# Kernel tuning notes

Hardware: AMD Instinct MI355X
Metric: run time of the kernel (lower is better)

Reference implementation:

```python
import jax, jax.numpy as jnp
import numpy as np

H, N_FULL, L_KERNEL, CHANNELS, RANK = 256, 128, 2048, 1, 1


def _legs_nplr(N, rank=1):
    # HiPPO-LegS transition + rank-1 correction -> NPLR (diag w - P P^*) form.
    q = np.arange(N, dtype=np.float64)
    col, row = np.meshgrid(q, q)
    r = 2 * q + 1
    M = -(np.where(row >= col, r, 0) - np.diag(q))
    T = np.sqrt(np.diag(2 * q + 1))
    A = T @ M @ np.linalg.inv(T)
    B = np.diag(T)                        # (N,)
    P = np.sqrt(0.5 + q)[None, :]         # (rank=1, N)
    AP = A + (P[:, :, None] * P[:, None, :]).sum(0)
    w, V = np.linalg.eig(AP)              # complex eigendecomposition
    w = w[0::2]                           # keep one of each conjugate pair -> N//2
    V = V[:, 0::2]
    V_inv = V.conj().T
    Bc = V_inv @ B.astype(V.dtype)        # (N//2,)
    Pc = (V_inv @ P.T.astype(V.dtype)).T  # (rank, N//2)
    return w, Pc, Bc


def _c2r(a):
    return jnp.stack([jnp.real(a), jnp.imag(a)], axis=-1).astype(jnp.float32)


def _r2c(a):
    return jax.lax.complex(a[..., 0], a[..., 1])


def setup_inputs() -> dict:
    key = jax.random.key(0)
    k1, k2 = jax.random.split(key)
    w, P, B = _legs_nplr(N_FULL, RANK)    # numpy complex128, half-size N = 64
    Nh = w.shape[-1]
    w = jnp.asarray(np.broadcast_to(w[None, :], (H, Nh)).copy())
    P = jnp.asarray(np.broadcast_to(P[:, None, :], (RANK, H, Nh)).copy())
    B = jnp.asarray(np.broadcast_to(B[None, None, :], (1, H, Nh)).copy())
    C = jax.random.normal(k1, (CHANNELS, H, Nh, 2), dtype=jnp.float32)
    log_dt = jax.random.uniform(k2, (H,), dtype=jnp.float32) * (
        float(np.log(0.1)) - float(np.log(0.001))) + float(np.log(0.001))
    return {
        'w_ri': _c2r(w), 'P_ri': _c2r(P), 'B_ri': _c2r(B),
        'C_ri': C, 'log_dt': log_dt, 'L': L_KERNEL,
    }


def reference(w_ri, P_ri, B_ri, C_ri, log_dt, L):
    w = _r2c(w_ri)        # (H, N) complex64
    P = _r2c(P_ri)        # (r, H, N)
    B = _r2c(B_ri)        # (1, H, N)
    C = _r2c(C_ri)        # (c, H, N)
    dt = jnp.exp(log_dt)  # (H,)
    Lh = L // 2 + 1
    # FFT nodes, processed through the bilinear transform
    omega = jnp.exp((-2j * np.pi / L) * jnp.arange(Lh, dtype=jnp.float32))
    z = 2 * (1 - omega) / (1 + omega)
    w_dt = w * dt[:, None]                               # incorporate dt into A
    Bcat = jnp.concatenate([B, P], axis=0)               # (1+r, H, N)
    Ccat = jnp.concatenate([C, jnp.conj(P)], axis=0)     # (c+r, H, N)  Q = conj(P)
    v = Bcat[:, None] * Ccat[None]                       # (1+r, c+r, H, N)
    # conjugate-symmetric extension to the full 2N poles
    v2 = jnp.concatenate([v, jnp.conj(v)], axis=-1)      # (1+r, c+r, H, 2N)
    w2 = jnp.concatenate([w_dt, jnp.conj(w_dt)], axis=-1)  # (H, 2N)
    # naive Cauchy sum (the O(N*L) hotspot): (1+r, c+r, H, Lh)
    r = (v2[..., None] / (z - w2[..., None])).sum(axis=-2)
    r = r * dt[None, None, :, None]
    # rank-1 Woodbury correction for the low-rank term
    k_f = r[:-1, :-1] - r[:-1, -1:] * r[-1:, :-1] / (1 + r[-1:, -1:])
    # final bilinear-transform correction, then frequency -> time
    k_f = k_f * 2 / (1 + omega)
    k = jnp.fft.irfft(k_f, n=L, axis=-1)                 # (1, c, H, L) real
    return k[0].astype(jnp.float32)                      # (c, H, L)
```

## Files before the change

### kernel.cpp

```cpp
#include <hip/hip_runtime.h>

#define NH 64
#define LFULL 2048
#define MH 1024
#define PI_F 3.14159265358979323846f
#define ANG_HALF 1.5339807878856412e-3f
#define ANG_3A   3.0679615757712823e-3f
#define ANG_FFT  6.1359231515425647e-3f

typedef __attribute__((ext_vector_type(2))) float f32x2;
typedef __attribute__((ext_vector_type(4))) float f32x4;

#define SV2(v, i, j) __builtin_shufflevector((v), (v), (i), (j))

#define ONE_POLE(SEL, pna, pm2, pa00, pb00, pa01, pb01, pa10, pb10, pa11, pb11) do { \
    f32x2 dr, di;                                                                    \
    asm("v_pk_add_f32 %0, %1, %2 op_sel:[" SEL ",0] op_sel_hi:[" SEL ",1]"           \
        : "=v"(dr) : "v"(pm2), "v"(nyy2));                                           \
    asm("v_pk_mul_f32 %0, %1, %2 op_sel:[" SEL ",0] op_sel_hi:[" SEL ",1]"           \
        : "=v"(di) : "v"(pna), "v"(yp));                                             \
    const f32x2 den = dr*dr + di*di;                                                 \
    const float pprod = den.x * den.y;                                               \
    const float ipp = __builtin_amdgcn_rcpf(pprod);                                  \
    f32x2 t;  t.x = ipp * den.y;  t.y = ipp * den.x;                                 \
    const f32x2 U = dr * t;                                                          \
    const f32x2 V = di * t;                                                          \
    asm("v_pk_fma_f32 %0, %1, %2, %0 op_sel:[" SEL ",0,0] op_sel_hi:[" SEL ",1,1]"   \
        : "+v"(s1_00) : "v"(pa00), "v"(U));                                          \
    asm("v_pk_fma_f32 %0, %1, %2, %0 op_sel:[" SEL ",0,0] op_sel_hi:[" SEL ",1,1]"   \
        : "+v"(s2_00) : "v"(pa00), "v"(V));                                          \
    asm("v_pk_fma_f32 %0, %1, %2, %0 op_sel:[" SEL ",0,0] op_sel_hi:[" SEL ",1,1]"   \
        : "+v"(s3_00) : "v"(pb00), "v"(U));                                          \
    asm("v_pk_fma_f32 %0, %1, %2, %0 op_sel:[" SEL ",0,0] op_sel_hi:[" SEL ",1,1]"   \
        : "+v"(s4_00) : "v"(pb00), "v"(V));                                          \
    asm("v_pk_fma_f32 %0, %1, %2, %0 op_sel:[" SEL ",0,0] op_sel_hi:[" SEL ",1,1]"   \
        : "+v"(s1_01) : "v"(pa01), "v"(U));                                          \
    asm("v_pk_fma_f32 %0, %1, %2, %0 op_sel:[" SEL ",0,0] op_sel_hi:[" SEL ",1,1]"   \
        : "+v"(s2_01) : "v"(pa01), "v"(V));                                          \
    asm("v_pk_fma_f32 %0, %1, %2, %0 op_sel:[" SEL ",0,0] op_sel_hi:[" SEL ",1,1]"   \
        : "+v"(s3_01) : "v"(pb01), "v"(U));                                          \
    asm("v_pk_fma_f32 %0, %1, %2, %0 op_sel:[" SEL ",0,0] op_sel_hi:[" SEL ",1,1]"   \
        : "+v"(s4_01) : "v"(pb01), "v"(V));                                          \
    asm("v_pk_fma_f32 %0, %1, %2, %0 op_sel:[" SEL ",0,0] op_sel_hi:[" SEL ",1,1]"   \
        : "+v"(s1_10) : "v"(pa10), "v"(U));                                          \
    asm("v_pk_fma_f32 %0, %1, %2, %0 op_sel:[" SEL ",0,0] op_sel_hi:[" SEL ",1,1]"   \
        : "+v"(s2_10) : "v"(pa10), "v"(V));                                          \
    asm("v_pk_fma_f32 %0, %1, %2, %0 op_sel:[" SEL ",0,0] op_sel_hi:[" SEL ",1,1]"   \
        : "+v"(s3_10) : "v"(pb10), "v"(U));                                          \
    asm("v_pk_fma_f32 %0, %1, %2, %0 op_sel:[" SEL ",0,0] op_sel_hi:[" SEL ",1,1]"   \
        : "+v"(s4_10) : "v"(pb10), "v"(V));                                          \
    asm("v_pk_fma_f32 %0, %1, %2, %0 op_sel:[" SEL ",0,0] op_sel_hi:[" SEL ",1,1]"   \
        : "+v"(s1_11) : "v"(pa11), "v"(U));                                          \
    asm("v_pk_fma_f32 %0, %1, %2, %0 op_sel:[" SEL ",0,0] op_sel_hi:[" SEL ",1,1]"   \
        : "+v"(s2_11) : "v"(pa11), "v"(V));                                          \
    asm("v_pk_fma_f32 %0, %1, %2, %0 op_sel:[" SEL ",0,0] op_sel_hi:[" SEL ",1,1]"   \
        : "+v"(s3_11) : "v"(pb11), "v"(U));                                          \
    asm("v_pk_fma_f32 %0, %1, %2, %0 op_sel:[" SEL ",0,0] op_sel_hi:[" SEL ",1,1]"   \
        : "+v"(s4_11) : "v"(pb11), "v"(V));                                          \
} while (0)

__global__ __launch_bounds__(512) void hippo_ssk(
    const float* __restrict__ w_ri,
    const float* __restrict__ P_ri,
    const float* __restrict__ B_ri,
    const float* __restrict__ C_ri,
    const float* __restrict__ log_dt,
    float* __restrict__ out)
{
    __shared__ __attribute__((aligned(16))) float coeff[10][NH];
    __shared__ float2 Kf[MH + 1];
    __shared__ float2 bufA[MH];
    __shared__ float2 bufB[MH];

    const int h    = blockIdx.x;
    const int tid  = threadIdx.x;
    const int c    = tid & 255;
    const int eps  = tid >> 8;

    float2 w_, P_, B_, C_;  float dtv = 0.f;
    if (tid < NH) {
        dtv = log_dt[h];
        w_ = ((const float2*)w_ri)[h*NH + tid];
        P_ = ((const float2*)P_ri)[h*NH + tid];
        B_ = ((const float2*)B_ri)[h*NH + tid];
        C_ = ((const float2*)C_ri)[h*NH + tid];
    }

    float shA, chA, shB, chB;
    __sincosf(ANG_HALF * (float)tid,         &shA, &chA);
    __sincosf(ANG_HALF * (float)(tid + 512), &shB, &chB);
    const float yA = 2.f * shA * __builtin_amdgcn_rcpf(chA);
    const float yB = 2.f * shB * __builtin_amdgcn_rcpf(chB);
    f32x2 yp;   yp.x = yA;        yp.y = yB;
    f32x2 nyy2; nyy2.x = -yA*yA;  nyy2.y = -yB*yB;
    float sa, ca;
    __sincosf(ANG_3A * (float)tid, &sa, &ca);
    const float cw0 = ca*ca - sa*sa;
    const float sw0 = 2.f*ca*sa;
    float w1c[4], w1s[4];
    #pragma unroll
    for (int mi = 0; mi < 4; ++mi) {
        const int m = 2 << (2*mi);
        __sincosf(ANG_FFT * (float)(c & ~(m-1)), &w1s[mi], &w1c[mi]);
    }

    if (tid < NH) {
        const float dt = __expf(dtv);
        const float a = w_.x * dt, b = w_.y * dt;
        const float v00r = (B_.x*C_.x - B_.y*C_.y) * dt;
        const float v00i = (B_.x*C_.y + B_.y*C_.x) * dt;
        const float v01r = (B_.x*P_.x + B_.y*P_.y) * dt;
        const float v01i = (B_.y*P_.x - B_.x*P_.y) * dt;
        const float v10r = (P_.x*C_.x - P_.y*C_.y) * dt;
        const float v10i = (P_.x*C_.y + P_.y*C_.x) * dt;
        const float v11  = (P_.x*P_.x + P_.y*P_.y) * dt;
        coeff[0][tid] = -2.f*a;
        coeff[1][tid] = fmaf(a, a, b*b);
        coeff[2][tid] = -2.f*fmaf(v00r, a, v00i*b);
        coeff[3][tid] = 2.f*v00r;
        coeff[4][tid] = -2.f*fmaf(v01r, a, v01i*b);
        coeff[5][tid] = 2.f*v01r;
        coeff[6][tid] = -2.f*fmaf(v10r, a, v10i*b);
        coeff[7][tid] = 2.f*v10r;
        coeff[8][tid] = -2.f*v11*a;
        coeff[9][tid] = 2.f*v11;
        float s = v00r;
        #pragma unroll
        for (int off = 32; off > 0; off >>= 1) s += __shfl_down(s, off, 64);
        if (tid == 0) Kf[MH] = make_float2(s, 0.f);
    }
    __syncthreads();

    {
        f32x2 s1_00={0,0}, s2_00={0,0}, s3_00={0,0}, s4_00={0,0};
        f32x2 s1_01={0,0}, s2_01={0,0}, s3_01={0,0}, s4_01={0,0};
        f32x2 s1_10={0,0}, s2_10={0,0}, s3_10={0,0}, s4_10={0,0};
        f32x2 s1_11={0,0}, s2_11={0,0}, s3_11={0,0}, s4_11={0,0};
        #pragma unroll 2
        for (int n = 0; n < NH; n += 4) {
            const f32x4 q0 = *reinterpret_cast<const f32x4*>(&coeff[0][n]);
            const f32x4 q1 = *reinterpret_cast<const f32x4*>(&coeff[1][n]);
            const f32x4 q2 = *reinterpret_cast<const f32x4*>(&coeff[2][n]);
            const f32x4 q3 = *reinterpret_cast<const f32x4*>(&coeff[3][n]);
            const f32x4 q4 = *reinterpret_cast<const f32x4*>(&coeff[4][n]);
            const f32x4 q5 = *reinterpret_cast<const f32x4*>(&coeff[5][n]);
            const f32x4 q6 = *reinterpret_cast<const f32x4*>(&coeff[6][n]);
            const f32x4 q7 = *reinterpret_cast<const f32x4*>(&coeff[7][n]);
            const f32x4 q8 = *reinterpret_cast<const f32x4*>(&coeff[8][n]);
            const f32x4 q9 = *reinterpret_cast<const f32x4*>(&coeff[9][n]);
            {
                const f32x2 pna = SV2(q0,0,1), pm2 = SV2(q1,0,1);
                const f32x2 pa00 = SV2(q2,0,1), pb00 = SV2(q3,0,1);
                const f32x2 pa01 = SV2(q4,0,1), pb01 = SV2(q5,0,1);
                const f32x2 pa10 = SV2(q6,0,1), pb10 = SV2(q7,0,1);
                const f32x2 pa11 = SV2(q8,0,1), pb11 = SV2(q9,0,1);
                ONE_POLE("0", pna, pm2, pa00, pb00, pa01, pb01, pa10, pb10, pa11, pb11);
                ONE_POLE("1", pna, pm2, pa00, pb00, pa01, pb01, pa10, pb10, pa11, pb11);
            }
            {
                const f32x2 pna = SV2(q0,2,3), pm2 = SV2(q1,2,3);
                const f32x2 pa00 = SV2(q2,2,3), pb00 = SV2(q3,2,3);
                const f32x2 pa01 = SV2(q4,2,3), pb01 = SV2(q5,2,3);
                const f32x2 pa10 = SV2(q6,2,3), pb10 = SV2(q7,2,3);
                const f32x2 pa11 = SV2(q8,2,3), pb11 = SV2(q9,2,3);
                ONE_POLE("0", pna, pm2, pa00, pb00, pa01, pb01, pa10, pb10, pa11, pb11);
                ONE_POLE("1", pna, pm2, pa00, pb00, pa01, pb01, pa10, pb10, pa11, pb11);
            }
        }
        const f32x2 r00r = yp*s4_00 + s1_00;
        const f32x2 r00i = yp*s3_00 - s2_00;
        const f32x2 r01r = yp*s4_01 + s1_01;
        const f32x2 r01i = yp*s3_01 - s2_01;
        const f32x2 r10r = yp*s4_10 + s1_10;
        const f32x2 r10i = yp*s3_10 - s2_10;
        const f32x2 r11r = yp*s4_11 + s1_11;
        const f32x2 r11i = yp*s3_11 - s2_11;
        const f32x2 nr = r01r*r10r - r01i*r10i;
        const f32x2 ni = r01r*r10i + r01i*r10r;
        const f32x2 dw = 1.f + r11r;
        const f32x2 dv = r11i;
        const f32x2 d2 = dw*dw + dv*dv;
        f32x2 id2;
        id2.x = __builtin_amdgcn_rcpf(d2.x);
        id2.y = __builtin_amdgcn_rcpf(d2.y);
        const f32x2 cr = (nr*dw + ni*dv)*id2;
        const f32x2 ci = (ni*dw - nr*dv)*id2;
        const f32x2 k0r = r00r - cr;
        const f32x2 k0i = r00i - ci;
        const f32x2 hy = 0.5f*yp;
        Kf[tid]       = make_float2(k0r.x - k0i.x*hy.x, k0i.x + k0r.x*hy.x);
        Kf[tid + 512] = make_float2(k0r.y - k0i.y*hy.y, k0i.y + k0r.y*hy.y);
    }
    __syncthreads();

    {
        float2 Xk = Kf[tid];
        if (tid == 0) Xk.y = 0.f;
        float2 Xc = Kf[MH - tid];  Xc.y = -Xc.y;
        const float Er0 = 0.5f*(Xk.x + Xc.x), Ei0 = 0.5f*(Xk.y + Xc.y);
        const float Tr0 = 0.5f*(Xk.x - Xc.x), Ti0 = 0.5f*(Xk.y - Xc.y);
        const float2 Z0 = make_float2(Er0 - (ca*Ti0 + sa*Tr0), Ei0 + (ca*Tr0 - sa*Ti0));
        const float2 Xk1 = Kf[tid + 512];
        float2 Xc1 = Kf[512 - tid];  Xc1.y = -Xc1.y;
        const float Er1 = 0.5f*(Xk1.x + Xc1.x), Ei1 = 0.5f*(Xk1.y + Xc1.y);
        const float Tr1 = 0.5f*(Xk1.x - Xc1.x), Ti1 = 0.5f*(Xk1.y - Xc1.y);
        const float Or1 = -sa*Tr1 - ca*Ti1;
        const float Oi1 = -sa*Ti1 + ca*Tr1;
        const float2 Z1 = make_float2(Er1 - Oi1, Ei1 + Or1);
        const float drr = Z0.x - Z1.x, dii = Z0.y - Z1.y;
        float4 outv;
        outv.x = Z0.x + Z1.x;
        outv.y = Z0.y + Z1.y;
        outv.z = cw0*drr - sw0*dii;
        outv.w = cw0*dii + sw0*drr;
        *reinterpret_cast<float4*>(&bufA[2*tid]) = outv;
    }
    __syncthreads();

    float2* Xb = bufA;
    float2* Yb = bufB;
    #pragma unroll
    for (int mi = 0; mi < 4; ++mi) {
        const int m   = 2 << (2*mi);
        const int jm1 = c & ~(m - 1);
        const int r   = c & (m - 1);
        const float c1v = w1c[mi], s1 = w1s[mi];
        const float2 x0 = Xb[c];
        const float2 x1 = Xb[c + 256];
        const float2 x2 = Xb[c + 512];
        const float2 x3 = Xb[c + 768];
        const float2 s02 = make_float2(x0.x + x2.x, x0.y + x2.y);
        const float2 d02 = make_float2(x0.x - x2.x, x0.y - x2.y);
        const float2 s13 = make_float2(x1.x + x3.x, x1.y + x3.y);
        const float2 d13 = make_float2(x1.x - x3.x, x1.y - x3.y);
        const float2 wd02 = make_float2(c1v*d02.x - s1*d02.y, c1v*d02.y + s1*d02.x);
        const float2 wd13 = make_float2(-s1*d13.x - c1v*d13.y, c1v*d13.x - s1*d13.y);
        const float2 Yu = eps ? wd02 : s02;
        const float2 Yv = eps ? wd13 : s13;
        const float Wc = c1v*c1v - s1*s1;
        const float Ws = 2.f*c1v*s1;
        const float2 Zp = make_float2(Yu.x + Yv.x, Yu.y + Yv.y);
        const float2 Zd = make_float2(Yu.x - Yv.x, Yu.y - Yv.y);
        const int p = 4*jm1 + (eps ? m : 0) + r;
        Yb[p]       = Zp;
        Yb[p + 2*m] = make_float2(Wc*Zd.x - Ws*Zd.y, Wc*Zd.y + Ws*Zd.x);
        __syncthreads();
        float2* t = Xb; Xb = Yb; Yb = t;
    }

    {
        const float sc = 1.0f/1024.0f;
        float2* op2 = (float2*)(out + (size_t)h * LFULL);
        const float2 a0 = Xb[tid];
        const float2 a1 = Xb[tid + 512];
        op2[tid]       = make_float2((a0.x + a1.x)*sc, (a0.y + a1.y)*sc);
        op2[tid + 512] = make_float2((a0.x - a1.x)*sc, (a0.y - a1.y)*sc);
    }
}

extern "C" void kernel_launch(void* const* d_in, const int* in_sizes, int n_in,
                              void* d_out, int out_size, void* d_ws, size_t ws_size,
                              hipStream_t stream) {
    const float* w_ri   = (const float*)d_in[0];
    const float* P_ri   = (const float*)d_in[1];
    const float* B_ri   = (const float*)d_in[2];
    const float* C_ri   = (const float*)d_in[3];
    const float* log_dt = (const float*)d_in[4];
    float* out = (float*)d_out;
    const int Hn = in_sizes[4];
    hippo_ssk<<<dim3(Hn), dim3(512), 0, stream>>>(w_ri, P_ri, B_ri, C_ri, log_dt, out);
}
```

Before: 15.69 us.

## Compute four frequencies per thread in Cauchy loop using half the block

The Cauchy sum is now done by only the first 256 threads, each handling four frequency nodes (two packed pairs) instead of two. Each coefficient LDS load is reused across twice as many frequencies, halving shared-memory read traffic for the pole loop. In exchange, half the block's waves sit idle during the dominant phase and per-thread register pressure doubles (64 accumulator registers), which may cut occupancy or cause spills. The loop unroll pragma is also dropped.

After: 21.12 us. 1.35x slower.

```diff
diff --git a/kernel.cpp b/kernel.cpp
--- a/kernel.cpp
+++ b/kernel.cpp
@@ -13,12 +13,12 @@
 
 #define SV2(v, i, j) __builtin_shufflevector((v), (v), (i), (j))
 
-#define ONE_POLE(SEL, pna, pm2, pa00, pb00, pa01, pb01, pa10, pb10, pa11, pb11) do { \
+#define ONE_POLE_G(SEL, G, YP, NYY2) do {                                            \
     f32x2 dr, di;                                                                    \
     asm("v_pk_add_f32 %0, %1, %2 op_sel:[" SEL ",0] op_sel_hi:[" SEL ",1]"           \
-        : "=v"(dr) : "v"(pm2), "v"(nyy2));                                           \
+        : "=v"(dr) : "v"(pm2), "v"(NYY2));                                           \
     asm("v_pk_mul_f32 %0, %1, %2 op_sel:[" SEL ",0] op_sel_hi:[" SEL ",1]"           \
-        : "=v"(di) : "v"(pna), "v"(yp));                                             \
+        : "=v"(di) : "v"(pna), "v"(YP));                                             \
     const f32x2 den = dr*dr + di*di;                                                 \
     const float pprod = den.x * den.y;                                               \
     const float ipp = __builtin_amdgcn_rcpf(pprod);                                  \
@@ -26,37 +26,63 @@
     const f32x2 U = dr * t;                                                          \
     const f32x2 V = di * t;                                                          \
     asm("v_pk_fma_f32 %0, %1, %2, %0 op_sel:[" SEL ",0,0] op_sel_hi:[" SEL ",1,1]"   \
-        : "+v"(s1_00) : "v"(pa00), "v"(U));                                          \
-    asm("v_pk_fma_f32 %0, %1, %2, %0 op_sel:[" SEL ",0,0] op_sel_hi:[" SEL ",1,1]"   \
-        : "+v"(s2_00) : "v"(pa00), "v"(V));                                          \
-    asm("v_pk_fma_f32 %0, %1, %2, %0 op_sel:[" SEL ",0,0] op_sel_hi:[" SEL ",1,1]"   \
-        : "+v"(s3_00) : "v"(pb00), "v"(U));                                          \
-    asm("v_pk_fma_f32 %0, %1, %2, %0 op_sel:[" SEL ",0,0] op_sel_hi:[" SEL ",1,1]"   \
-        : "+v"(s4_00) : "v"(pb00), "v"(V));                                          \
-    asm("v_pk_fma_f32 %0, %1, %2, %0 op_sel:[" SEL ",0,0] op_sel_hi:[" SEL ",1,1]"   \
-        : "+v"(s1_01) : "v"(pa01), "v"(U));                                          \
-    asm("v_pk_fma_f32 %0, %1, %2, %0 op_sel:[" SEL ",0,0] op_sel_hi:[" SEL ",1,1]"   \
-        : "+v"(s2_01) : "v"(pa01), "v"(V));                                          \
-    asm("v_pk_fma_f32 %0, %1, %2, %0 op_sel:[" SEL ",0,0] op_sel_hi:[" SEL ",1,1]"   \
-        : "+v"(s3_01) : "v"(pb01), "v"(U));                                          \
-    asm("v_pk_fma_f32 %0, %1, %2, %0 op_sel:[" SEL ",0,0] op_sel_hi:[" SEL ",1,1]"   \
-        : "+v"(s4_01) : "v"(pb01), "v"(V));                                          \
-    asm("v_pk_fma_f32 %0, %1, %2, %0 op_sel:[" SEL ",0,0] op_sel_hi:[" SEL ",1,1]"   \
-        : "+v"(s1_10) : "v"(pa10), "v"(U));                                          \
-    asm("v_pk_fma_f32 %0, %1, %2, %0 op_sel:[" SEL ",0,0] op_sel_hi:[" SEL ",1,1]"   \
-        : "+v"(s2_10) : "v"(pa10), "v"(V));                                          \
-    asm("v_pk_fma_f32 %0, %1, %2, %0 op_sel:[" SEL ",0,0] op_sel_hi:[" SEL ",1,1]"   \
-        : "+v"(s3_10) : "v"(pb10), "v"(U));                                          \
-    asm("v_pk_fma_f32 %0, %1, %2, %0 op_sel:[" SEL ",0,0] op_sel_hi:[" SEL ",1,1]"   \
-        : "+v"(s4_10) : "v"(pb10), "v"(V));                                          \
-    asm("v_pk_fma_f32 %0, %1, %2, %0 op_sel:[" SEL ",0,0] op_sel_hi:[" SEL ",1,1]"   \
-        : "+v"(s1_11) : "v"(pa11), "v"(U));                                          \
-    asm("v_pk_fma_f32 %0, %1, %2, %0 op_sel:[" SEL ",0,0] op_sel_hi:[" SEL ",1,1]"   \
-        : "+v"(s2_11) : "v"(pa11), "v"(V));                                          \
-    asm("v_pk_fma_f32 %0, %1, %2, %0 op_sel:[" SEL ",0,0] op_sel_hi:[" SEL ",1,1]"   \
-        : "+v"(s3_11) : "v"(pb11), "v"(U));                                          \
-    asm("v_pk_fma_f32 %0, %1, %2, %0 op_sel:[" SEL ",0,0] op_sel_hi:[" SEL ",1,1]"   \
-        : "+v"(s4_11) : "v"(pb11), "v"(V));                                          \
+        : "+v"(s1_00##G) : "v"(pa00), "v"(U));                                       \
+    asm("v_pk_fma_f32 %0, %1, %2, %0 op_sel:[" SEL ",0,0] op_sel_hi:[" SEL ",1,1]"   \
+        : "+v"(s2_00##G) : "v"(pa00), "v"(V));                                       \
+    asm("v_pk_fma_f32 %0, %1, %2, %0 op_sel:[" SEL ",0,0] op_sel_hi:[" SEL ",1,1]"   \
+        : "+v"(s3_00##G) : "v"(pb00), "v"(U));                                       \
+    asm("v_pk_fma_f32 %0, %1, %2, %0 op_sel:[" SEL ",0,0] op_sel_hi:[" SEL ",1,1]"   \
+        : "+v"(s4_00##G) : "v"(pb00), "v"(V));                                       \
+    asm("v_pk_fma_f32 %0, %1, %2, %0 op_sel:[" SEL ",0,0] op_sel_hi:[" SEL ",1,1]"   \
+        : "+v"(s1_01##G) : "v"(pa01), "v"(U));                                       \
+    asm("v_pk_fma_f32 %0, %1, %2, %0 op_sel:[" SEL ",0,0] op_sel_hi:[" SEL ",1,1]"   \
+        : "+v"(s2_01##G) : "v"(pa01), "v"(V));                                       \
+    asm("v_pk_fma_f32 %0, %1, %2, %0 op_sel:[" SEL ",0,0] op_sel_hi:[" SEL ",1,1]"   \
+        : "+v"(s3_01##G) : "v"(pb01), "v"(U));                                       \
+    asm("v_pk_fma_f32 %0, %1, %2, %0 op_sel:[" SEL ",0,0] op_sel_hi:[" SEL ",1,1]"   \
+        : "+v"(s4_01##G) : "v"(pb01), "v"(V));                                       \
+    asm("v_pk_fma_f32 %0, %1, %2, %0 op_sel:[" SEL ",0,0] op_sel_hi:[" SEL ",1,1]"   \
+        : "+v"(s1_10##G) : "v"(pa10), "v"(U));                                       \
+    asm("v_pk_fma_f32 %0, %1, %2, %0 op_sel:[" SEL ",0,0] op_sel_hi:[" SEL ",1,1]"   \
+        : "+v"(s2_10##G) : "v"(pa10), "v"(V));                                       \
+    asm("v_pk_fma_f32 %0, %1, %2, %0 op_sel:[" SEL ",0,0] op_sel_hi:[" SEL ",1,1]"   \
+        : "+v"(s3_10##G) : "v"(pb10), "v"(U));                                       \
+    asm("v_pk_fma_f32 %0, %1, %2, %0 op_sel:[" SEL ",0,0] op_sel_hi:[" SEL ",1,1]"   \
+        : "+v"(s4_10##G) : "v"(pb10), "v"(V));                                       \
+    asm("v_pk_fma_f32 %0, %1, %2, %0 op_sel:[" SEL ",0,0] op_sel_hi:[" SEL ",1,1]"   \
+        : "+v"(s1_11##G) : "v"(pa11), "v"(U));                                       \
+    asm("v_pk_fma_f32 %0, %1, %2, %0 op_sel:[" SEL ",0,0] op_sel_hi:[" SEL ",1,1]"   \
+        : "+v"(s2_11##G) : "v"(pa11), "v"(V));                                       \
+    asm("v_pk_fma_f32 %0, %1, %2, %0 op_sel:[" SEL ",0,0] op_sel_hi:[" SEL ",1,1]"   \
+        : "+v"(s3_11##G) : "v"(pb11), "v"(U));                                       \
+    asm("v_pk_fma_f32 %0, %1, %2, %0 op_sel:[" SEL ",0,0] op_sel_hi:[" SEL ",1,1]"   \
+        : "+v"(s4_11##G) : "v"(pb11), "v"(V));                                       \
+} while (0)
+
+#define FINISH_G(G, YP, L0, L1) do {                                                 \
+    const f32x2 r00r = (YP)*s4_00##G + s1_00##G;                                     \
+    const f32x2 r00i = (YP)*s3_00##G - s2_00##G;                                     \
+    const f32x2 r01r = (YP)*s4_01##G + s1_01##G;                                     \
+    const f32x2 r01i = (YP)*s3_01##G - s2_01##G;                                     \
+    const f32x2 r10r = (YP)*s4_10##G + s1_10##G;                                     \
+    const f32x2 r10i = (YP)*s3_10##G - s2_10##G;                                     \
+    const f32x2 r11r = (YP)*s4_11##G + s1_11##G;                                     \
+    const f32x2 r11i = (YP)*s3_11##G - s2_11##G;                                     \
+    const f32x2 nr = r01r*r10r - r01i*r10i;                                          \
+    const f32x2 ni = r01r*r10i + r01i*r10r;                                          \
+    const f32x2 dw = 1.f + r11r;                                                     \
+    const f32x2 dv = r11i;                                                           \
+    const f32x2 d2 = dw*dw + dv*dv;                                                  \
+    f32x2 id2;                                                                       \
+    id2.x = __builtin_amdgcn_rcpf(d2.x);                                             \
+    id2.y = __builtin_amdgcn_rcpf(d2.y);                                             \
+    const f32x2 cr = (nr*dw + ni*dv)*id2;                                            \
+    const f32x2 ci = (ni*dw - nr*dv)*id2;                                            \
+    const f32x2 k0r = r00r - cr;                                                     \
+    const f32x2 k0i = r00i - ci;                                                     \
+    const f32x2 hy = 0.5f*(YP);                                                      \
+    Kf[(L0)] = make_float2(k0r.x - k0i.x*hy.x, k0i.x + k0r.x*hy.x);                  \
+    Kf[(L1)] = make_float2(k0r.y - k0i.y*hy.y, k0i.y + k0r.y*hy.y);                  \
 } while (0)
 
 __global__ __launch_bounds__(512) void hippo_ssk(
@@ -86,13 +112,20 @@
         C_ = ((const float2*)C_ri)[h*NH + tid];
     }
 
-    float shA, chA, shB, chB;
-    __sincosf(ANG_HALF * (float)tid,         &shA, &chA);
-    __sincosf(ANG_HALF * (float)(tid + 512), &shB, &chB);
-    const float yA = 2.f * shA * __builtin_amdgcn_rcpf(chA);
-    const float yB = 2.f * shB * __builtin_amdgcn_rcpf(chB);
-    f32x2 yp;   yp.x = yA;        yp.y = yB;
-    f32x2 nyy2; nyy2.x = -yA*yA;  nyy2.y = -yB*yB;
+    f32x2 ypA, nyy2A, ypB, nyy2B;
+    {
+        float sh0, ch0, sh1, ch1, sh2, ch2, sh3, ch3;
+        __sincosf(ANG_HALF * (float)c,         &sh0, &ch0);
+        __sincosf(ANG_HALF * (float)(c + 512), &sh1, &ch1);
+        __sincosf(ANG_HALF * (float)(c + 256), &sh2, &ch2);
+        __sincosf(ANG_HALF * (float)(c + 768), &sh3, &ch3);
+        const float y0 = 2.f * sh0 * __builtin_amdgcn_rcpf(ch0);
+        const float y1 = 2.f * sh1 * __builtin_amdgcn_rcpf(ch1);
+        const float y2 = 2.f * sh2 * __builtin_amdgcn_rcpf(ch2);
+        const float y3 = 2.f * sh3 * __builtin_amdgcn_rcpf(ch3);
+        ypA.x = y0;  ypA.y = y1;  nyy2A.x = -y0*y0;  nyy2A.y = -y1*y1;
+        ypB.x = y2;  ypB.y = y3;  nyy2B.x = -y2*y2;  nyy2B.y = -y3*y3;
+    }
     float sa, ca;
     __sincosf(ANG_3A * (float)tid, &sa, &ca);
     const float cw0 = ca*ca - sa*sa;
@@ -131,12 +164,15 @@
     }
     __syncthreads();
 
-    {
-        f32x2 s1_00={0,0}, s2_00={0,0}, s3_00={0,0}, s4_00={0,0};
-        f32x2 s1_01={0,0}, s2_01={0,0}, s3_01={0,0}, s4_01={0,0};
-        f32x2 s1_10={0,0}, s2_10={0,0}, s3_10={0,0}, s4_10={0,0};
-        f32x2 s1_11={0,0}, s2_11={0,0}, s3_11={0,0}, s4_11={0,0};
-        #pragma unroll 2
+    if (tid < 256) {
+        f32x2 s1_00A={0,0}, s2_00A={0,0}, s3_00A={0,0}, s4_00A={0,0};
+        f32x2 s1_01A={0,0}, s2_01A={0,0}, s3_01A={0,0}, s4_01A={0,0};
+        f32x2 s1_10A={0,0}, s2_10A={0,0}, s3_10A={0,0}, s4_10A={0,0};
+        f32x2 s1_11A={0,0}, s2_11A={0,0}, s3_11A={0,0}, s4_11A={0,0};
+        f32x2 s1_00B={0,0}, s2_00B={0,0}, s3_00B={0,0}, s4_00B={0,0};
+        f32x2 s1_01B={0,0}, s2_01B={0,0}, s3_01B={0,0}, s4_01B={0,0};
+        f32x2 s1_10B={0,0}, s2_10B={0,0}, s3_10B={0,0}, s4_10B={0,0};
+        f32x2 s1_11B={0,0}, s2_11B={0,0}, s3_11B={0,0}, s4_11B={0,0};
         for (int n = 0; n < NH; n += 4) {
             const f32x4 q0 = *reinterpret_cast<const f32x4*>(&coeff[0][n]);
             const f32x4 q1 = *reinterpret_cast<const f32x4*>(&coeff[1][n]);
@@ -154,8 +190,10 @@
                 const f32x2 pa01 = SV2(q4,0,1), pb01 = SV2(q5,0,1);
                 const f32x2 pa10 = SV2(q6,0,1), pb10 = SV2(q7,0,1);
                 const f32x2 pa11 = SV2(q8,0,1), pb11 = SV2(q9,0,1);
-                ONE_POLE("0", pna, pm2, pa00, pb00, pa01, pb01, pa10, pb10, pa11, pb11);
-                ONE_POLE("1", pna, pm2, pa00, pb00, pa01, pb01, pa10, pb10, pa11, pb11);
+                ONE_POLE_G("0", A, ypA, nyy2A);
+                ONE_POLE_G("0", B, ypB, nyy2B);
+                ONE_POLE_G("1", A, ypA, nyy2A);
+                ONE_POLE_G("1", B, ypB, nyy2B);
             }
             {
                 const f32x2 pna = SV2(q0,2,3), pm2 = SV2(q1,2,3);
@@ -163,33 +201,14 @@
                 const f32x2 pa01 = SV2(q4,2,3), pb01 = SV2(q5,2,3);
                 const f32x2 pa10 = SV2(q6,2,3), pb10 = SV2(q7,2,3);
                 const f32x2 pa11 = SV2(q8,2,3), pb11 = SV2(q9,2,3);
-                ONE_POLE("0", pna, pm2, pa00, pb00, pa01, pb01, pa10, pb10, pa11, pb11);
-                ONE_POLE("1", pna, pm2, pa00, pb00, pa01, pb01, pa10, pb10, pa11, pb11);
+                ONE_POLE_G("0", A, ypA, nyy2A);
+                ONE_POLE_G("0", B, ypB, nyy2B);
+                ONE_POLE_G("1", A, ypA, nyy2A);
+                ONE_POLE_G("1", B, ypB, nyy2B);
             }
         }
-        const f32x2 r00r = yp*s4_00 + s1_00;
-        const f32x2 r00i = yp*s3_00 - s2_00;
-        const f32x2 r01r = yp*s4_01 + s1_01;
-        const f32x2 r01i = yp*s3_01 - s2_01;
-        const f32x2 r10r = yp*s4_10 + s1_10;
-        const f32x2 r10i = yp*s3_10 - s2_10;
-        const f32x2 r11r = yp*s4_11 + s1_11;
-        const f32x2 r11i = yp*s3_11 - s2_11;
-        const f32x2 nr = r01r*r10r - r01i*r10i;
-        const f32x2 ni = r01r*r10i + r01i*r10r;
-        const f32x2 dw = 1.f + r11r;
-        const f32x2 dv = r11i;
-        const f32x2 d2 = dw*dw + dv*dv;
-        f32x2 id2;
-        id2.x = __builtin_amdgcn_rcpf(d2.x);
-        id2.y = __builtin_amdgcn_rcpf(d2.y);
-        const f32x2 cr = (nr*dw + ni*dv)*id2;
-        const f32x2 ci = (ni*dw - nr*dv)*id2;
-        const f32x2 k0r = r00r - cr;
-        const f32x2 k0i = r00i - ci;
-        const f32x2 hy = 0.5f*yp;
-        Kf[tid]       = make_float2(k0r.x - k0i.x*hy.x, k0i.x + k0r.x*hy.x);
-        Kf[tid + 512] = make_float2(k0r.y - k0i.y*hy.y, k0i.y + k0r.y*hy.y);
+        FINISH_G(A, ypA, c,       c + 512);
+        FINISH_G(B, ypB, c + 256, c + 768);
     }
     __syncthreads();
 
```
